# Kernel tuning notes

Hardware: AMD Instinct MI355X
Metric: run time of the kernel (lower is better)

The kernel has to match this reference:

```python
import jax, jax.numpy as jnp
import numpy as np

STRIDE, PADDING, EPS = 2, 1, 1e-5


def setup_inputs() -> dict:
    key = jax.random.key(0)
    k1, k2, k3 = jax.random.split(key, 3)
    C_in, C_out, K = 64, 64, 4
    x = jax.random.normal(k1, (32, C_in, 64, 64), dtype=jnp.float32)
    weight = jax.random.normal(k2, (C_in, C_out, K, K), dtype=jnp.float32) * 0.05  # torch layout (in,out,kh,kw)
    conv_bias = jax.random.normal(k3, (C_out,), dtype=jnp.float32) * 0.02
    gamma = jnp.ones((C_out,), dtype=jnp.float32)
    beta = jnp.zeros((C_out,), dtype=jnp.float32)
    running_mean = jnp.zeros((C_out,), dtype=jnp.float32)
    running_var = jnp.ones((C_out,), dtype=jnp.float32)
    return {"x": x, "weight": weight, "conv_bias": conv_bias, "gamma": gamma,
            "beta": beta, "running_mean": running_mean, "running_var": running_var}


def _conv_transpose2d(x, weight, bias, stride, padding):
    # torch.nn.functional.conv_transpose2d equivalent:
    # conv with lhs_dilation=stride, spatially-flipped kernel, in/out axes swapped,
    # and padding k-1-p on each side.
    k = weight.shape[2]
    w_t = jnp.transpose(jnp.flip(weight, (2, 3)), (1, 0, 2, 3))  # (Cout, Cin, k, k)
    pad = k - 1 - padding
    y = jax.lax.conv_general_dilated(
        x, w_t,
        window_strides=(1, 1),
        padding=[(pad, pad), (pad, pad)],
        lhs_dilation=(stride, stride),
        dimension_numbers=("NCHW", "OIHW", "NCHW"),
    )
    return y + bias[None, :, None, None]


def reference(x, weight, conv_bias, gamma, beta, running_mean, running_var):
    # ConvTranspose2d
    y = _conv_transpose2d(x, weight, conv_bias, STRIDE, PADDING)  # [N,C,128,128]
    # BatchNorm2d (inference, running stats)
    scale = gamma * jax.lax.rsqrt(running_var + EPS)
    y = (y - running_mean[None, :, None, None]) * scale[None, :, None, None] + beta[None, :, None, None]
    # Softmax over channel dim
    y = jax.nn.softmax(y, axis=1)
    # MaxPool2d(k=2, s=2): H,W are even, so reshape-max is exact
    N, C, H, W = y.shape
    y = y.reshape(N, C, H // 2, 2, W // 2, 2).max(axis=(3, 5))  # [N,C,64,64]
    return y
```

## Files before the change

### kernel.cpp

```cpp
#include <hip/hip_runtime.h>
#include <hip/hip_bf16.h>
#include <math.h>


typedef __attribute__((ext_vector_type(8))) short short8;
typedef __attribute__((ext_vector_type(4))) float floatx4;
typedef __attribute__((ext_vector_type(2))) unsigned uint2v;

__device__ ushort g_wfrag[4 * 8 * 4 * 64 * 8];
__device__ float g_aff[64];

#define L2E 1.44269504088896340736f

__device__ __forceinline__ ushort f2bf(float f) {
  union { float f; unsigned u; } v; v.f = f;
  unsigned r = v.u + 0x7FFF + ((v.u >> 16) & 1);
  return (ushort)(r >> 16);
}

__global__ __launch_bounds__(256) void prep_kernel(
    const float* __restrict__ w, const float* __restrict__ bias,
    const float* __restrict__ gamma, const float* __restrict__ beta,
    const float* __restrict__ mean, const float* __restrict__ var) {
  int t = blockIdx.x * 256 + threadIdx.x;
  int cin0 = (t >> 6) * 2;
  int cout = t & 63;
  int nt = cout >> 4, b15 = cout & 15;
  int q = (cin0 & 31) >> 3;
  int j = cin0 & 7;
  int ksq = cin0 >> 5;
  float Aw = gamma[cout] * rsqrtf(var[cout] + 1e-5f) * L2E;

  const float4* p0 = (const float4*)&w[(cin0 * 64 + cout) * 16];
  const float4* p1 = (const float4*)&w[((cin0 + 1) * 64 + cout) * 16];
  float a[16], b[16];
  {
    float4 f0 = p0[0], f1 = p0[1], f2 = p0[2], f3 = p0[3];
    a[0]=f0.x; a[1]=f0.y; a[2]=f0.z; a[3]=f0.w; a[4]=f1.x; a[5]=f1.y; a[6]=f1.z; a[7]=f1.w;
    a[8]=f2.x; a[9]=f2.y; a[10]=f2.z; a[11]=f2.w; a[12]=f3.x; a[13]=f3.y; a[14]=f3.z; a[15]=f3.w;
    float4 g0 = p1[0], g1 = p1[1], g2 = p1[2], g3 = p1[3];
    b[0]=g0.x; b[1]=g0.y; b[2]=g0.z; b[3]=g0.w; b[4]=g1.x; b[5]=g1.y; b[6]=g1.z; b[7]=g1.w;
    b[8]=g2.x; b[9]=g2.y; b[10]=g2.z; b[11]=g2.w; b[12]=g3.x; b[13]=g3.y; b[14]=g3.z; b[15]=g3.w;
  }
#pragma unroll
  for (int kh = 0; kh < 4; ++kh)
#pragma unroll
    for (int kw = 0; kw < 4; ++kw) {
      int r = (kh & 1) ? 0 : 1;
      int pp = (kw & 1) ? 0 : 1;
      int c = r * 2 + pp;
      int tap = (kh >> 1) * 2 + (kw >> 1);
      int ks = tap * 2 + ksq;
      unsigned u = (unsigned)f2bf(a[kh * 4 + kw] * Aw) |
                   ((unsigned)f2bf(b[kh * 4 + kw] * Aw) << 16);
      *(unsigned*)&g_wfrag[(((c * 8 + ks) * 4 + nt) * 64 + q * 16 + b15) * 8 + j] = u;
    }

  if (t < 64) {
    float A0 = gamma[t] * rsqrtf(var[t] + 1e-5f);
    g_aff[t] = ((bias[t] - mean[t]) * A0 + beta[t]) * L2E;
  }
}

__device__ __forceinline__ unsigned cvtpk(float a, float b) {
  unsigned r;
  asm("v_cvt_pk_bf16_f32 %0, %1, %2" : "=v"(r) : "v"(a), "v"(b));
  return r;
}

template <int CTRL>
__device__ __forceinline__ float dpp_add(float v) {
  unsigned t = (unsigned)__builtin_amdgcn_update_dpp(
      0, (int)__float_as_uint(v), CTRL, 0xF, 0xF, true);
  return v + __uint_as_float(t);
}

__device__ __forceinline__ float sum16(float v) {
  v = dpp_add<0xB1>(v);
  v = dpp_add<0x4E>(v);
  v = dpp_add<0x141>(v);
  v = dpp_add<0x140>(v);
  return v;
}

__device__ __forceinline__ float fexp2(float x) {
#if __has_builtin(__builtin_amdgcn_exp2f)
  return __builtin_amdgcn_exp2f(x);
#else
  return exp2f(x);
#endif
}

#define COLS 66
#define ROWSTRIDE (COLS * 64)

__global__ __launch_bounds__(512, 4) void fused_kernel(const float* __restrict__ x,
                                                       float* __restrict__ out) {
  __shared__ __align__(16) ushort xs[4 * ROWSTRIDE];
  __shared__ __align__(16) float red[2 * 64 * 65 + 16];

  const int tid  = threadIdx.x;
  const int swz  = ((blockIdx.x & 7) << 2) | (blockIdx.x >> 3);
  const int ph0  = swz * 2;
  const int n    = blockIdx.y;
  const int wave = tid >> 6;
  const int lane = tid & 63;
  const int b15  = lane & 15;
  const int q    = lane >> 4;
  const int wc   = wave & 1;
  const int c    = wave >> 1;
  const int r    = c >> 1, p = c & 1;

  short8 bfA[4], bfB[4];
  {
    const short8* wf = (const short8*)g_wfrag + (c * 8) * 256;
#pragma unroll
    for (int nt = 0; nt < 4; ++nt) bfA[nt] = wf[nt * 64 + lane];
  }

  {
    float4 z = {0.f, 0.f, 0.f, 0.f};
    for (int e = tid; e < 2084; e += 512) ((float4*)red)[e] = z;
  }

  for (int e = tid; e < 1024; e += 512) {
    int iw4 = e & 15;
    int c4  = (e >> 4) & 15;
    int row = e >> 8;
    int ih  = ph0 - 1 + row;
    float4 v0 = {0.f, 0.f, 0.f, 0.f}, v1 = v0, v2 = v0, v3 = v0;
    if (ih >= 0 && ih < 64) {
      const float* xp = x + ((n * 64 + c4 * 4) * 64 + ih) * 64 + iw4 * 4;
      v0 = *(const float4*)xp;          v1 = *(const float4*)(xp + 4096);
      v2 = *(const float4*)(xp + 8192); v3 = *(const float4*)(xp + 12288);
    }
    int chunk = c4 >> 1, half4 = (c4 & 1) * 4;
    float cc[4][4] = {{v0.x, v1.x, v2.x, v3.x}, {v0.y, v1.y, v2.y, v3.y},
                      {v0.z, v1.z, v2.z, v3.z}, {v0.w, v1.w, v2.w, v3.w}};
#pragma unroll
    for (int ii = 0; ii < 4; ++ii) {
      int col = iw4 * 4 + ii + 1;
      uint2v pk = {cvtpk(cc[ii][0], cc[ii][1]), cvtpk(cc[ii][2], cc[ii][3])};
      *(uint2v*)&xs[(row * COLS + col) * 64 + ((chunk ^ (col & 7)) * 8) + half4] = pk;
    }
  }
  for (int e = tid; e < 128; e += 512) {
    int c4 = e & 15, side = (e >> 4) & 1, row = e >> 5;
    int col = side ? 65 : 0;
    int chunk = c4 >> 1, half4 = (c4 & 1) * 4;
    ushort4 z; z.x = z.y = z.z = z.w = 0;
    *(ushort4*)&xs[(row * COLS + col) * 64 + ((chunk ^ (col & 7)) * 8) + half4] = z;
  }

  float Dc[4];
#pragma unroll
  for (int nt = 0; nt < 4; ++nt) Dc[nt] = g_aff[nt * 16 + b15];

  int A2[2][2];
#pragma unroll
  for (int b = 0; b < 2; ++b) {
    int col = wc * 32 + b15 + (b ? p - 1 : p) + 1;
#pragma unroll
    for (int par = 0; par < 2; ++par)
      A2[b][par] = r * ROWSTRIDE + col * 64 + (((par * 4 + q) ^ (col & 7)) * 8);
  }

  __syncthreads();

  floatx4 acc[16];
#pragma unroll
  for (int i = 0; i < 16; ++i) {
    float d = Dc[i & 3];
    acc[i] = (floatx4){d, d, d, d};
  }

#pragma unroll
  for (int ks = 0; ks < 8; ++ks) {
    short8* bcur = (ks & 1) ? bfB : bfA;
    short8* bnxt = (ks & 1) ? bfA : bfB;
    if (ks < 7) {
      const short8* wf = (const short8*)g_wfrag + (c * 8 + ks + 1) * 256;
#pragma unroll
      for (int nt = 0; nt < 4; ++nt) bnxt[nt] = wf[nt * 64 + lane];
    }
    const int b_ = (ks >> 1) & 1, par_ = ks & 1;
    const int ro = (ks >> 2) ? 0 : ROWSTRIDE;
    const int base = A2[b_][par_] + ro;
    short8 af00 = *(const short8*)&xs[base];
    short8 af01 = *(const short8*)&xs[base + 1024];
    short8 af10 = *(const short8*)&xs[base + ROWSTRIDE];
    short8 af11 = *(const short8*)&xs[base + ROWSTRIDE + 1024];
#pragma unroll
    for (int nt = 0; nt < 4; ++nt) {
      acc[nt]      = __builtin_amdgcn_mfma_f32_16x16x32_bf16(af00, bcur[nt], acc[nt], 0, 0, 0);
      acc[4 + nt]  = __builtin_amdgcn_mfma_f32_16x16x32_bf16(af01, bcur[nt], acc[4 + nt], 0, 0, 0);
      acc[8 + nt]  = __builtin_amdgcn_mfma_f32_16x16x32_bf16(af10, bcur[nt], acc[8 + nt], 0, 0, 0);
      acc[12 + nt] = __builtin_amdgcn_mfma_f32_16x16x32_bf16(af11, bcur[nt], acc[12 + nt], 0, 0, 0);
    }
  }

#pragma unroll
  for (int prow = 0; prow < 2; ++prow)
#pragma unroll
    for (int mt = 0; mt < 2; ++mt) {
      float sm[4] = {0.f, 0.f, 0.f, 0.f};
#pragma unroll
      for (int nt = 0; nt < 4; ++nt)
#pragma unroll
        for (int reg = 0; reg < 4; ++reg) {
          float e = fexp2(acc[prow * 8 + mt * 4 + nt][reg]);
          acc[prow * 8 + mt * 4 + nt][reg] = e;
          sm[reg] += e;
        }
#pragma unroll
      for (int reg = 0; reg < 4; ++reg)
        sm[reg] = __builtin_amdgcn_rcpf(sum16(sm[reg]));
#pragma unroll
      for (int nt = 0; nt < 4; ++nt) {
        int idx = (prow * 64 + nt * 16 + b15) * 65 + wc * 32 + mt * 16 + q * 4;
#pragma unroll
        for (int reg = 0; reg < 4; ++reg) {
          float v = acc[prow * 8 + mt * 4 + nt][reg] * sm[reg];
          __hip_atomic_fetch_max((unsigned*)&red[idx + reg], __float_as_uint(v),
                                 __ATOMIC_RELAXED, __HIP_MEMORY_SCOPE_WORKGROUP);
        }
      }
    }
  __syncthreads();

  for (int e = tid; e < 4096; e += 512) {
    int pw2  = e & 31;
    int cout = (e >> 5) & 63;
    int rl   = e >> 11;
    int base = (rl * 64 + cout) * 65 + pw2 * 2;
    float2 val = {red[base], red[base + 1]};
    *(float2*)&out[((n * 64 + cout) * 64 + (ph0 + rl)) * 64 + pw2 * 2] = val;
  }
}

extern "C" void kernel_launch(void* const* d_in, const int* in_sizes, int n_in,
                              void* d_out, int out_size, void* d_ws, size_t ws_size,
                              hipStream_t stream) {
  const float* x     = (const float*)d_in[0];
  const float* w     = (const float*)d_in[1];
  const float* bias  = (const float*)d_in[2];
  const float* gamma = (const float*)d_in[3];
  const float* beta  = (const float*)d_in[4];
  const float* mean  = (const float*)d_in[5];
  const float* var   = (const float*)d_in[6];
  float* out = (float*)d_out;

  prep_kernel<<<8, 256, 0, stream>>>(w, bias, gamma, beta, mean, var);
  dim3 grid(32, 32);
  fused_kernel<<<grid, 512, 0, stream>>>(x, out);
}
```

Measured before the change: 124.9 us.

## Stream weight fragments into an LDS double buffer via global_load_lds

Weight B-fragments were prefetched from global memory into a register double buffer. They are now copied straight into a per-wave LDS double buffer with global_load_lds, then read back from LDS before the MFMAs. A full vmcnt wait sits at the top of each k-step, and the occupancy hint in launch bounds drops from 4 to 2. The aim is to cut register pressure and overlap weight staging with compute. In exchange the kernel needs an extra 64 KB of LDS, which roughly halves the number of resident blocks per CU.

New measurement: 117.8 us. -5.7%, faster.

```diff
diff --git a/kernel.cpp b/kernel.cpp
--- a/kernel.cpp
+++ b/kernel.cpp
@@ -91,12 +91,19 @@
 #endif
 }
 
+__device__ __forceinline__ void gload_lds16(const void* g, void* l) {
+  __builtin_amdgcn_global_load_lds(
+      (const __attribute__((address_space(1))) void*)g,
+      (__attribute__((address_space(3))) void*)l, 16, 0, 0);
+}
+
 #define COLS 66
 #define ROWSTRIDE (COLS * 64)
 
-__global__ __launch_bounds__(512, 4) void fused_kernel(const float* __restrict__ x,
+__global__ __launch_bounds__(512, 2) void fused_kernel(const float* __restrict__ x,
                                                        float* __restrict__ out) {
   __shared__ __align__(16) ushort xs[4 * ROWSTRIDE];
+  __shared__ __align__(16) ushort wbuf[2 * 8 * 4 * 512];
   __shared__ __align__(16) float red[2 * 64 * 65 + 16];
 
   const int tid  = threadIdx.x;
@@ -111,12 +118,14 @@
   const int c    = wave >> 1;
   const int r    = c >> 1, p = c & 1;
 
-  short8 bfA[4], bfB[4];
-  {
-    const short8* wf = (const short8*)g_wfrag + (c * 8) * 256;
-#pragma unroll
-    for (int nt = 0; nt < 4; ++nt) bfA[nt] = wf[nt * 64 + lane];
-  }
+#define STAGE_W(buf_, ks_)                                                    \
+  {                                                                           \
+    _Pragma("unroll")                                                         \
+    for (int nt_ = 0; nt_ < 4; ++nt_)                                         \
+      gload_lds16(&g_wfrag[(((c * 8 + (ks_)) * 4 + nt_) * 64 + lane) * 8],    \
+                  &wbuf[(((buf_)*8 + wave) * 4 + nt_) * 512]);                \
+  }
+  STAGE_W(0, 0);
 
   {
     float4 z = {0.f, 0.f, 0.f, 0.f};
@@ -176,13 +185,12 @@
 
 #pragma unroll
   for (int ks = 0; ks < 8; ++ks) {
-    short8* bcur = (ks & 1) ? bfB : bfA;
-    short8* bnxt = (ks & 1) ? bfA : bfB;
-    if (ks < 7) {
-      const short8* wf = (const short8*)g_wfrag + (c * 8 + ks + 1) * 256;
-#pragma unroll
-      for (int nt = 0; nt < 4; ++nt) bnxt[nt] = wf[nt * 64 + lane];
-    }
+    const int cur = ks & 1;
+    asm volatile("s_waitcnt vmcnt(0)" ::: "memory");
+    short8 bf[4];
+#pragma unroll
+    for (int nt = 0; nt < 4; ++nt)
+      bf[nt] = *(const short8*)&wbuf[((cur * 8 + wave) * 4 + nt) * 512 + lane * 8];
     const int b_ = (ks >> 1) & 1, par_ = ks & 1;
     const int ro = (ks >> 2) ? 0 : ROWSTRIDE;
     const int base = A2[b_][par_] + ro;
@@ -190,12 +198,13 @@
     short8 af01 = *(const short8*)&xs[base + 1024];
     short8 af10 = *(const short8*)&xs[base + ROWSTRIDE];
     short8 af11 = *(const short8*)&xs[base + ROWSTRIDE + 1024];
+    if (ks < 7) STAGE_W(cur ^ 1, ks + 1);
 #pragma unroll
     for (int nt = 0; nt < 4; ++nt) {
-      acc[nt]      = __builtin_amdgcn_mfma_f32_16x16x32_bf16(af00, bcur[nt], acc[nt], 0, 0, 0);
-      acc[4 + nt]  = __builtin_amdgcn_mfma_f32_16x16x32_bf16(af01, bcur[nt], acc[4 + nt], 0, 0, 0);
-      acc[8 + nt]  = __builtin_amdgcn_mfma_f32_16x16x32_bf16(af10, bcur[nt], acc[8 + nt], 0, 0, 0);
-      acc[12 + nt] = __builtin_amdgcn_mfma_f32_16x16x32_bf16(af11, bcur[nt], acc[12 + nt], 0, 0, 0);
+      acc[nt]      = __builtin_amdgcn_mfma_f32_16x16x32_bf16(af00, bf[nt], acc[nt], 0, 0, 0);
+      acc[4 + nt]  = __builtin_amdgcn_mfma_f32_16x16x32_bf16(af01, bf[nt], acc[4 + nt], 0, 0, 0);
+      acc[8 + nt]  = __builtin_amdgcn_mfma_f32_16x16x32_bf16(af10, bf[nt], acc[8 + nt], 0, 0, 0);
+      acc[12 + nt] = __builtin_amdgcn_mfma_f32_16x16x32_bf16(af11, bf[nt], acc[12 + nt], 0, 0, 0);
     }
   }
 
```
